# Optimization experiments

Measured on AMD Instinct MI355X. Metric: run time of the kernel, lower is better.

## Reference

```python
import jax, jax.numpy as jnp
import numpy as np

TOPK = 2
ALPHA_AUX = 0.02

def setup_inputs() -> dict:
    key = jax.random.key(0)
    ks = jax.random.split(key, 6)
    B, T, D, E, H = 2, 2048, 1024, 16, 1536
    s_in = 1.0 / np.sqrt(D)
    s_h = 1.0 / np.sqrt(H)
    return {
        "x": jax.random.normal(ks[0], (B, T, D), dtype=jnp.float32),
        "router_w": jax.random.normal(ks[1], (E, D), dtype=jnp.float32) * s_in,
        "w1": jax.random.normal(ks[2], (E, H, D), dtype=jnp.float32) * s_in,
        "b1": jax.random.normal(ks[3], (E, H), dtype=jnp.float32) * 0.01,
        "w2": jax.random.normal(ks[4], (E, D, H), dtype=jnp.float32) * s_h,
        "b2": jax.random.normal(ks[5], (E, D), dtype=jnp.float32) * 0.01,
    }

def reference(x, router_w, w1, b1, w2, b2):
    B, T, D = x.shape
    E = router_w.shape[0]
    N = B * T
    x_flat = x.reshape(N, D)

    # Router: top-k logits -> softmax gates -> dense dispatch matrix [N, E]
    logits = x_flat @ router_w.T                      # [N, E]
    vals, idx = jax.lax.top_k(logits, TOPK)           # [N, K]
    gate = jax.nn.softmax(vals, axis=-1)              # [N, K]
    rows = jnp.arange(N)[:, None]
    dispatch = jnp.zeros((N, E), dtype=x.dtype).at[rows, idx].set(gate)

    # Expert MLPs computed densely over all experts; gate==0 masks unselected,
    # reproducing the gather-MLP-scatter math exactly.
    h = jnp.einsum('nd,ehd->neh', x_flat, w1) + b1    # [N, E, H]
    h = jax.nn.gelu(h, approximate=True)              # tanh GELU
    y = jnp.einsum('neh,edh->ned', h, w2) + b2        # [N, E, D]
    out = jnp.einsum('ne,ned->nd', dispatch, y).reshape(B, T, D)

    # Auxiliary load-balancing loss
    tok_per_expert = (dispatch > 0).sum(0).astype(jnp.float32)  # [E]
    f_i = tok_per_expert / tok_per_expert.sum()
    m_i = dispatch.sum(0) / jnp.clip(tok_per_expert, 1.0, None)
    aux_loss = ALPHA_AUX * (f_i * m_i).mean()
    return out, aux_loss
```

## Files before the change

kernel.cpp:

```cpp
#include <hip/hip_runtime.h>
#include <hip/hip_bf16.h>
#include <math.h>

#define N_TOK 4096
#define DIM   1024
#define NEXP  16
#define HID   1536
#define TOPK2 2
#define NASSIGN (N_TOK * TOPK2)

#define MAX_ITEMS 80

typedef __attribute__((ext_vector_type(8))) short short8;
typedef __attribute__((ext_vector_type(4))) float floatx4;
typedef unsigned short u16;

#define GLOAD_LDS16(gp, lp)                                                     \
    __builtin_amdgcn_global_load_lds(                                           \
        (const __attribute__((address_space(1))) unsigned int*)(gp),            \
        (__attribute__((address_space(3))) unsigned int*)(lp), 16, 0, 0)

__global__ void cvt_kernel(const float* __restrict__ src, u16* __restrict__ dst, int n4) {
    int i = blockIdx.x * 256 + threadIdx.x;
    if (i >= n4) return;
    float4 v = ((const float4*)src)[i];
    __hip_bfloat16 a = __float2bfloat16(v.x), b = __float2bfloat16(v.y);
    __hip_bfloat16 c = __float2bfloat16(v.z), d = __float2bfloat16(v.w);
    ushort4 o;
    o.x = *(u16*)&a; o.y = *(u16*)&b; o.z = *(u16*)&c; o.w = *(u16*)&d;
    ((ushort4*)dst)[i] = o;
}

__global__ __launch_bounds__(256)
void logits_topk_kernel(const float* __restrict__ x, const float* __restrict__ rw,
                        int* __restrict__ idx, float* __restrict__ gate) {
    int tb = blockIdx.x * 16;
    __shared__ float xs[16][68];
    __shared__ float rs[16][68];
    __shared__ float lg[16][17];

    int tid = threadIdx.x;
    int t = tid >> 4, e = tid & 15;
    int srow = tid >> 4, scol = (tid & 15) * 4;

    float acc = 0.f;
    for (int k0 = 0; k0 < DIM; k0 += 64) {
        *(float4*)&xs[srow][scol] = *(const float4*)&x[(size_t)(tb + srow) * DIM + k0 + scol];
        *(float4*)&rs[srow][scol] = *(const float4*)&rw[(size_t)srow * DIM + k0 + scol];
        __syncthreads();
        const float2* xp = (const float2*)xs[t];
        const float2* rp = (const float2*)rs[e];
        #pragma unroll
        for (int k = 0; k < 32; k++) {
            float2 a = xp[k], b = rp[k];
            acc = fmaf(a.x, b.x, acc);
            acc = fmaf(a.y, b.y, acc);
        }
        __syncthreads();
    }
    lg[t][e] = acc;
    __syncthreads();

    if (tid < 16) {
        int n = tb + tid;
        float v0 = -3.402823466e+38f, v1 = -3.402823466e+38f;
        int i0 = 0, i1 = 0;
        #pragma unroll
        for (int ee = 0; ee < NEXP; ee++) {
            float v = lg[tid][ee];
            if (v > v0) { v1 = v0; i1 = i0; v0 = v; i0 = ee; }
            else if (v > v1) { v1 = v; i1 = ee; }
        }
        float e1 = expf(v1 - v0);
        float inv = 1.f / (1.f + e1);
        idx[2 * n] = i0; idx[2 * n + 1] = i1;
        gate[2 * n] = inv; gate[2 * n + 1] = e1 * inv;
    }
}

__global__ __launch_bounds__(256)
void plan_kernel(const int* __restrict__ idx, const float* __restrict__ gate,
                 int* __restrict__ offsets, int* __restrict__ tlist,
                 int* __restrict__ wl, int* __restrict__ wcount,
                 float* __restrict__ aux_out) {
    __shared__ int cnt_s[16];
    __shared__ float gs_s[16];
    __shared__ int pos_s[16];
    __shared__ int offs_s[17];
    int tid = threadIdx.x;
    if (tid < 16) { cnt_s[tid] = 0; gs_s[tid] = 0.f; pos_s[tid] = 0; }
    __syncthreads();
    for (int i = tid; i < NASSIGN; i += 256) {
        int e = idx[i];
        atomicAdd(&cnt_s[e], 1);
        atomicAdd(&gs_s[e], gate[i]);
    }
    __syncthreads();
    if (tid == 0) {
        int acc = 0;
        for (int e = 0; e < NEXP; e++) { offs_s[e] = acc; acc += cnt_s[e]; }
        offs_s[NEXP] = acc;
        float tot = (float)acc;
        float s = 0.f;
        for (int e = 0; e < NEXP; e++) {
            float c = (float)cnt_s[e];
            s += (c / tot) * (gs_s[e] / fmaxf(c, 1.f));
        }
        *aux_out = 0.02f * (s / (float)NEXP);
        int m = 0;
        for (int e = 0; e < NEXP; e++) {
            int nt = (cnt_s[e] + 127) >> 7;
            for (int rt = 0; rt < nt; rt++) wl[m++] = (e << 8) | rt;
        }
        *wcount = m;
    }
    __syncthreads();
    if (tid < 17) offsets[tid] = offs_s[tid];
    for (int i = tid; i < NASSIGN; i += 256) {
        int e = idx[i];
        int p = atomicAdd(&pos_s[e], 1);
        tlist[offs_s[e] + p] = i;
    }
}

__device__ __forceinline__ float gelu_tanh(float v) {
    float v3 = v * v * v;
    float t = tanhf(0.7978845608028654f * (v + 0.044715f * v3));
    return 0.5f * v * (1.f + t);
}


__global__ __launch_bounds__(256)
void gemm1_kernel(const u16* __restrict__ xb, const u16* __restrict__ w1b,
                  const float* __restrict__ b1,
                  const int* __restrict__ offsets, const int* __restrict__ tlist,
                  const int* __restrict__ wl, const int* __restrict__ wcount,
                  u16* __restrict__ h_bf) {
    int bid = blockIdx.x;
    int item = bid / 12;
    if (item >= *wcount) return;
    int colt = bid - item * 12;
    int w = wl[item];
    int e = w >> 8, rt = w & 255;
    int beg = offsets[e], ne = offsets[e + 1] - beg;
    int row0 = rt * 128, col0 = colt * 128;

    __shared__ u16 As[128 * 32];
    __shared__ u16 Bs[128 * 32];

    int tid = threadIdx.x;
    int wave = tid >> 6, lane = tid & 63;
    int wm = wave & 1, wn = wave >> 1;

    int koff = (((lane & 3) ^ ((lane >> 3) & 3)) * 8);
    const u16* aptr[2];
    const u16* bptr[2];
    #pragma unroll
    for (int q = 0; q < 2; q++) {
        int lrow = wave * 32 + q * 16 + (lane >> 2);
        int gi = beg + row0 + lrow;
        int gi2 = (row0 + lrow < ne) ? gi : beg;
        int tok = tlist[gi2] >> 1;
        aptr[q] = xb + (size_t)tok * DIM + koff;
        int n = col0 + lrow;
        bptr[q] = w1b + (size_t)(e * HID + n) * DIM + koff;
    }

    int rchunk = (((lane >> 4) ^ ((lane >> 1) & 3)) * 8);

    floatx4 acc[4][4] = {};
    for (int k0 = 0; k0 < DIM; k0 += 32) {
        #pragma unroll
        for (int q = 0; q < 2; q++) {
            GLOAD_LDS16(aptr[q] + k0, &As[(wave * 32 + q * 16) * 32]);
            GLOAD_LDS16(bptr[q] + k0, &Bs[(wave * 32 + q * 16) * 32]);
        }
        __syncthreads();
        short8 af[4], bf_[4];
        #pragma unroll
        for (int mi = 0; mi < 4; mi++)
            af[mi] = *(const short8*)&As[(wm * 64 + mi * 16 + (lane & 15)) * 32 + rchunk];
        #pragma unroll
        for (int nj = 0; nj < 4; nj++)
            bf_[nj] = *(const short8*)&Bs[(wn * 64 + nj * 16 + (lane & 15)) * 32 + rchunk];
        #pragma unroll
        for (int mi = 0; mi < 4; mi++)
            #pragma unroll
            for (int nj = 0; nj < 4; nj++)
                acc[mi][nj] = __builtin_amdgcn_mfma_f32_16x16x32_bf16(af[mi], bf_[nj], acc[mi][nj], 0, 0, 0);
        __syncthreads();
    }

    #pragma unroll
    for (int mi = 0; mi < 4; mi++) {
        #pragma unroll
        for (int r = 0; r < 4; r++) {
            int lrow = wm * 64 + mi * 16 + (lane >> 4) * 4 + r;
            if (row0 + lrow >= ne) continue;
            size_t orow = (size_t)(beg + row0 + lrow);
            #pragma unroll
            for (int nj = 0; nj < 4; nj++) {
                int col = col0 + wn * 64 + nj * 16 + (lane & 15);
                float v = acc[mi][nj][r] + b1[e * HID + col];
                __hip_bfloat16 hb = __float2bfloat16(gelu_tanh(v));
                h_bf[orow * HID + col] = *(u16*)&hb;
            }
        }
    }
}

__global__ __launch_bounds__(256)
void gemm2_kernel(const u16* __restrict__ h_bf, const u16* __restrict__ w2b,
                  const float* __restrict__ b2,
                  const int* __restrict__ offsets, const int* __restrict__ tlist,
                  const int* __restrict__ wl, const int* __restrict__ wcount,
                  const float* __restrict__ gate, float* __restrict__ out) {
    int bid = blockIdx.x;
    int item = bid >> 3;
    if (item >= *wcount) return;
    int colt = bid & 7;
    int w = wl[item];
    int e = w >> 8, rt = w & 255;
    int beg = offsets[e], ne = offsets[e + 1] - beg;
    int row0 = rt * 128, col0 = colt * 128;

    __shared__ u16 As[128 * 32];
    __shared__ u16 Bs[128 * 32];

    int tid = threadIdx.x;
    int wave = tid >> 6, lane = tid & 63;
    int wm = wave & 1, wn = wave >> 1;

    int koff = (((lane & 3) ^ ((lane >> 3) & 3)) * 8);
    const u16* aptr[2];
    const u16* bptr[2];
    #pragma unroll
    for (int q = 0; q < 2; q++) {
        int lrow = wave * 32 + q * 16 + (lane >> 2);
        int gi = beg + row0 + lrow;
        int gi2 = (row0 + lrow < ne) ? gi : beg;
        aptr[q] = h_bf + (size_t)gi2 * HID + koff;
        int n = col0 + lrow;
        bptr[q] = w2b + (size_t)(e * DIM + n) * HID + koff;
    }

    int rchunk = (((lane >> 4) ^ ((lane >> 1) & 3)) * 8);

    floatx4 acc[4][4] = {};
    for (int k0 = 0; k0 < HID; k0 += 32) {
        #pragma unroll
        for (int q = 0; q < 2; q++) {
            GLOAD_LDS16(aptr[q] + k0, &As[(wave * 32 + q * 16) * 32]);
            GLOAD_LDS16(bptr[q] + k0, &Bs[(wave * 32 + q * 16) * 32]);
        }
        __syncthreads();
        short8 af[4], bf_[4];
        #pragma unroll
        for (int mi = 0; mi < 4; mi++)
            af[mi] = *(const short8*)&As[(wm * 64 + mi * 16 + (lane & 15)) * 32 + rchunk];
        #pragma unroll
        for (int nj = 0; nj < 4; nj++)
            bf_[nj] = *(const short8*)&Bs[(wn * 64 + nj * 16 + (lane & 15)) * 32 + rchunk];
        #pragma unroll
        for (int mi = 0; mi < 4; mi++)
            #pragma unroll
            for (int nj = 0; nj < 4; nj++)
                acc[mi][nj] = __builtin_amdgcn_mfma_f32_16x16x32_bf16(af[mi], bf_[nj], acc[mi][nj], 0, 0, 0);
        __syncthreads();
    }

    #pragma unroll
    for (int mi = 0; mi < 4; mi++) {
        #pragma unroll
        for (int r = 0; r < 4; r++) {
            int lrow = wm * 64 + mi * 16 + (lane >> 4) * 4 + r;
            if (row0 + lrow >= ne) continue;
            int t = tlist[beg + row0 + lrow];
            float g = gate[t];
            int tok = t >> 1;
            #pragma unroll
            for (int nj = 0; nj < 4; nj++) {
                int col = col0 + wn * 64 + nj * 16 + (lane & 15);
                float v = g * (acc[mi][nj][r] + b2[e * DIM + col]);
                atomicAdd(&out[(size_t)tok * DIM + col], v);
            }
        }
    }
}

extern "C" void kernel_launch(void* const* d_in, const int* in_sizes, int n_in,
                              void* d_out, int out_size, void* d_ws, size_t ws_size,
                              hipStream_t stream) {
    const float* x  = (const float*)d_in[0];
    const float* rw = (const float*)d_in[1];
    const float* w1 = (const float*)d_in[2];
    const float* b1 = (const float*)d_in[3];
    const float* w2 = (const float*)d_in[4];
    const float* b2 = (const float*)d_in[5];
    float* out = (float*)d_out;

    char* ws = (char*)d_ws;
    int*   offsets = (int*)(ws + 192);
    int*   wcount  = (int*)(ws + 384);
    int*   wl      = (int*)(ws + 512);
    int*   idx     = (int*)(ws + 4096);
    float* gate    = (float*)(ws + 4096 + 4 * NASSIGN);
    int*   tlist   = (int*)(ws + 4096 + 8 * NASSIGN);
    u16*   x_bf    = (u16*)(ws + (128 << 10));
    u16*   h_bf    = x_bf + (size_t)N_TOK * DIM;
    u16*   w_bf    = h_bf + (size_t)NASSIGN * HID;

    hipMemsetAsync(d_out, 0, (size_t)out_size * 4, stream);

    cvt_kernel<<<(N_TOK * DIM / 4 + 255) / 256, 256, 0, stream>>>(x, x_bf, N_TOK * DIM / 4);
    cvt_kernel<<<(NEXP * HID * DIM / 4 + 255) / 256, 256, 0, stream>>>(w1, w_bf, NEXP * HID * DIM / 4);

    logits_topk_kernel<<<N_TOK / 16, 256, 0, stream>>>(x, rw, idx, gate);
    plan_kernel<<<1, 256, 0, stream>>>(idx, gate, offsets, tlist, wl, wcount,
                                       out + (size_t)N_TOK * DIM);

    gemm1_kernel<<<MAX_ITEMS * 12, 256, 0, stream>>>(
        x_bf, w_bf, b1, offsets, tlist, wl, wcount, h_bf);

    cvt_kernel<<<(NEXP * DIM * HID / 4 + 255) / 256, 256, 0, stream>>>(w2, w_bf, NEXP * DIM * HID / 4);

    gemm2_kernel<<<MAX_ITEMS * 8, 256, 0, stream>>>(
        h_bf, w_bf, b2, offsets, tlist, wl, wcount, gate, out);
}
```

Baseline: 455.7 us.

## Double-buffer GEMM LDS tiles, split-K gemm2, fuse x conversion into router

Both expert GEMMs now use two LDS buffers, so the next K-tile's global-to-LDS load is issued while MFMAs run on the current tile. gemm2 is split in half along the hidden dimension, doubling its block count; the bias is added only by the first half and both halves accumulate into the output atomically. The separate x-to-bf16 conversion kernel is removed and the conversion is done inside the router logits kernel, which already reads x. The cost is twice the LDS per block and twice the atomic traffic on the output in gemm2.

```diff
diff --git a/kernel.cpp b/kernel.cpp
--- a/kernel.cpp
+++ b/kernel.cpp
@@ -33,7 +33,8 @@
 
 __global__ __launch_bounds__(256)
 void logits_topk_kernel(const float* __restrict__ x, const float* __restrict__ rw,
-                        int* __restrict__ idx, float* __restrict__ gate) {
+                        int* __restrict__ idx, float* __restrict__ gate,
+                        u16* __restrict__ x_bf) {
     int tb = blockIdx.x * 16;
     __shared__ float xs[16][68];
     __shared__ float rs[16][68];
@@ -45,8 +46,16 @@
 
     float acc = 0.f;
     for (int k0 = 0; k0 < DIM; k0 += 64) {
-        *(float4*)&xs[srow][scol] = *(const float4*)&x[(size_t)(tb + srow) * DIM + k0 + scol];
+        float4 xv = *(const float4*)&x[(size_t)(tb + srow) * DIM + k0 + scol];
+        *(float4*)&xs[srow][scol] = xv;
         *(float4*)&rs[srow][scol] = *(const float4*)&rw[(size_t)srow * DIM + k0 + scol];
+        {
+            __hip_bfloat16 a = __float2bfloat16(xv.x), b = __float2bfloat16(xv.y);
+            __hip_bfloat16 c = __float2bfloat16(xv.z), d = __float2bfloat16(xv.w);
+            ushort4 o;
+            o.x = *(u16*)&a; o.y = *(u16*)&b; o.z = *(u16*)&c; o.w = *(u16*)&d;
+            *(ushort4*)&x_bf[(size_t)(tb + srow) * DIM + k0 + scol] = o;
+        }
         __syncthreads();
         const float2* xp = (const float2*)xs[t];
         const float2* rp = (const float2*)rs[e];
@@ -145,8 +154,8 @@
     int beg = offsets[e], ne = offsets[e + 1] - beg;
     int row0 = rt * 128, col0 = colt * 128;
 
-    __shared__ u16 As[128 * 32];
-    __shared__ u16 Bs[128 * 32];
+    __shared__ u16 As[2][128 * 32];
+    __shared__ u16 Bs[2][128 * 32];
 
     int tid = threadIdx.x;
     int wave = tid >> 6, lane = tid & 63;
@@ -169,26 +178,35 @@
     int rchunk = (((lane >> 4) ^ ((lane >> 1) & 3)) * 8);
 
     floatx4 acc[4][4] = {};
+    #pragma unroll
+    for (int q = 0; q < 2; q++) {
+        GLOAD_LDS16(aptr[q], &As[0][(wave * 32 + q * 16) * 32]);
+        GLOAD_LDS16(bptr[q], &Bs[0][(wave * 32 + q * 16) * 32]);
+    }
+    __syncthreads();
+    int cur = 0;
     for (int k0 = 0; k0 < DIM; k0 += 32) {
-        #pragma unroll
-        for (int q = 0; q < 2; q++) {
-            GLOAD_LDS16(aptr[q] + k0, &As[(wave * 32 + q * 16) * 32]);
-            GLOAD_LDS16(bptr[q] + k0, &Bs[(wave * 32 + q * 16) * 32]);
-        }
-        __syncthreads();
+        if (k0 + 32 < DIM) {
+            #pragma unroll
+            for (int q = 0; q < 2; q++) {
+                GLOAD_LDS16(aptr[q] + k0 + 32, &As[cur ^ 1][(wave * 32 + q * 16) * 32]);
+                GLOAD_LDS16(bptr[q] + k0 + 32, &Bs[cur ^ 1][(wave * 32 + q * 16) * 32]);
+            }
+        }
         short8 af[4], bf_[4];
         #pragma unroll
         for (int mi = 0; mi < 4; mi++)
-            af[mi] = *(const short8*)&As[(wm * 64 + mi * 16 + (lane & 15)) * 32 + rchunk];
+            af[mi] = *(const short8*)&As[cur][(wm * 64 + mi * 16 + (lane & 15)) * 32 + rchunk];
         #pragma unroll
         for (int nj = 0; nj < 4; nj++)
-            bf_[nj] = *(const short8*)&Bs[(wn * 64 + nj * 16 + (lane & 15)) * 32 + rchunk];
+            bf_[nj] = *(const short8*)&Bs[cur][(wn * 64 + nj * 16 + (lane & 15)) * 32 + rchunk];
         #pragma unroll
         for (int mi = 0; mi < 4; mi++)
             #pragma unroll
             for (int nj = 0; nj < 4; nj++)
                 acc[mi][nj] = __builtin_amdgcn_mfma_f32_16x16x32_bf16(af[mi], bf_[nj], acc[mi][nj], 0, 0, 0);
         __syncthreads();
+        cur ^= 1;
     }
 
     #pragma unroll
@@ -216,16 +234,19 @@
                   const int* __restrict__ wl, const int* __restrict__ wcount,
                   const float* __restrict__ gate, float* __restrict__ out) {
     int bid = blockIdx.x;
-    int item = bid >> 3;
+    int item = bid >> 4;
     if (item >= *wcount) return;
     int colt = bid & 7;
+    int ks = (bid >> 3) & 1;
     int w = wl[item];
     int e = w >> 8, rt = w & 255;
     int beg = offsets[e], ne = offsets[e + 1] - beg;
     int row0 = rt * 128, col0 = colt * 128;
-
-    __shared__ u16 As[128 * 32];
-    __shared__ u16 Bs[128 * 32];
+    int kbeg = ks * (HID / 2);
+    int kend = kbeg + (HID / 2);
+
+    __shared__ u16 As[2][128 * 32];
+    __shared__ u16 Bs[2][128 * 32];
 
     int tid = threadIdx.x;
     int wave = tid >> 6, lane = tid & 63;
@@ -247,26 +268,35 @@
     int rchunk = (((lane >> 4) ^ ((lane >> 1) & 3)) * 8);
 
     floatx4 acc[4][4] = {};
-    for (int k0 = 0; k0 < HID; k0 += 32) {
-        #pragma unroll
-        for (int q = 0; q < 2; q++) {
-            GLOAD_LDS16(aptr[q] + k0, &As[(wave * 32 + q * 16) * 32]);
-            GLOAD_LDS16(bptr[q] + k0, &Bs[(wave * 32 + q * 16) * 32]);
-        }
-        __syncthreads();
+    #pragma unroll
+    for (int q = 0; q < 2; q++) {
+        GLOAD_LDS16(aptr[q] + kbeg, &As[0][(wave * 32 + q * 16) * 32]);
+        GLOAD_LDS16(bptr[q] + kbeg, &Bs[0][(wave * 32 + q * 16) * 32]);
+    }
+    __syncthreads();
+    int cur = 0;
+    for (int k0 = kbeg; k0 < kend; k0 += 32) {
+        if (k0 + 32 < kend) {
+            #pragma unroll
+            for (int q = 0; q < 2; q++) {
+                GLOAD_LDS16(aptr[q] + k0 + 32, &As[cur ^ 1][(wave * 32 + q * 16) * 32]);
+                GLOAD_LDS16(bptr[q] + k0 + 32, &Bs[cur ^ 1][(wave * 32 + q * 16) * 32]);
+            }
+        }
         short8 af[4], bf_[4];
         #pragma unroll
         for (int mi = 0; mi < 4; mi++)
-            af[mi] = *(const short8*)&As[(wm * 64 + mi * 16 + (lane & 15)) * 32 + rchunk];
+            af[mi] = *(const short8*)&As[cur][(wm * 64 + mi * 16 + (lane & 15)) * 32 + rchunk];
         #pragma unroll
         for (int nj = 0; nj < 4; nj++)
-            bf_[nj] = *(const short8*)&Bs[(wn * 64 + nj * 16 + (lane & 15)) * 32 + rchunk];
+            bf_[nj] = *(const short8*)&Bs[cur][(wn * 64 + nj * 16 + (lane & 15)) * 32 + rchunk];
         #pragma unroll
         for (int mi = 0; mi < 4; mi++)
             #pragma unroll
             for (int nj = 0; nj < 4; nj++)
                 acc[mi][nj] = __builtin_amdgcn_mfma_f32_16x16x32_bf16(af[mi], bf_[nj], acc[mi][nj], 0, 0, 0);
         __syncthreads();
+        cur ^= 1;
     }
 
     #pragma unroll
@@ -281,7 +311,9 @@
             #pragma unroll
             for (int nj = 0; nj < 4; nj++) {
                 int col = col0 + wn * 64 + nj * 16 + (lane & 15);
-                float v = g * (acc[mi][nj][r] + b2[e * DIM + col]);
+                float v = acc[mi][nj][r];
+                if (ks == 0) v += b2[e * DIM + col];
+                v *= g;
                 atomicAdd(&out[(size_t)tok * DIM + col], v);
             }
         }
@@ -312,10 +344,9 @@
 
     hipMemsetAsync(d_out, 0, (size_t)out_size * 4, stream);
 
-    cvt_kernel<<<(N_TOK * DIM / 4 + 255) / 256, 256, 0, stream>>>(x, x_bf, N_TOK * DIM / 4);
     cvt_kernel<<<(NEXP * HID * DIM / 4 + 255) / 256, 256, 0, stream>>>(w1, w_bf, NEXP * HID * DIM / 4);
 
-    logits_topk_kernel<<<N_TOK / 16, 256, 0, stream>>>(x, rw, idx, gate);
+    logits_topk_kernel<<<N_TOK / 16, 256, 0, stream>>>(x, rw, idx, gate, x_bf);
     plan_kernel<<<1, 256, 0, stream>>>(idx, gate, offsets, tlist, wl, wcount,
                                        out + (size_t)N_TOK * DIM);
 
@@ -324,6 +355,6 @@
 
     cvt_kernel<<<(NEXP * DIM * HID / 4 + 255) / 256, 256, 0, stream>>>(w2, w_bf, NEXP * DIM * HID / 4);
 
-    gemm2_kernel<<<MAX_ITEMS * 8, 256, 0, stream>>>(
+    gemm2_kernel<<<MAX_ITEMS * 16, 256, 0, stream>>>(
         h_bf, w_bf, b2, offsets, tlist, wl, wcount, gate, out);
 }
```

Result: slower. 487.1 us (+6.9%).

## Fuse weight bf16 conversion into GEMMs, double-buffer LDS, replace atomics with combine

Applied to the files above, without the earlier changes.

Drops the separate fp32-to-bf16 conversion passes over w1 and w2. The GEMM kernels now load the fp32 weights directly, convert them in registers and write swizzled bf16 tiles into double-buffered shared memory, so the next tile's loads overlap the MFMA work. The conversion of x to bf16 moves into the router kernel. gemm2 writes gated per-slot outputs to a buffer, and a new combine kernel sums each token's two slots, which replaces the output memset and the float atomics. In exchange, every block re-reads and re-converts the fp32 weights, which doubles weight bytes per tile, and an extra fp32 y buffer is written and read back.

```diff
diff --git a/kernel.cpp b/kernel.cpp
--- a/kernel.cpp
+++ b/kernel.cpp
@@ -10,6 +10,8 @@
 #define NASSIGN (N_TOK * TOPK2)
 
 #define MAX_ITEMS 80
+#define G1_BLOCKS (MAX_ITEMS * 12)
+#define G2_BLOCKS (MAX_ITEMS * 8)
 
 typedef __attribute__((ext_vector_type(8))) short short8;
 typedef __attribute__((ext_vector_type(4))) float floatx4;
@@ -20,33 +22,43 @@
         (const __attribute__((address_space(1))) unsigned int*)(gp),            \
         (__attribute__((address_space(3))) unsigned int*)(lp), 16, 0, 0)
 
-__global__ void cvt_kernel(const float* __restrict__ src, u16* __restrict__ dst, int n4) {
-    int i = blockIdx.x * 256 + threadIdx.x;
-    if (i >= n4) return;
-    float4 v = ((const float4*)src)[i];
-    __hip_bfloat16 a = __float2bfloat16(v.x), b = __float2bfloat16(v.y);
-    __hip_bfloat16 c = __float2bfloat16(v.z), d = __float2bfloat16(v.w);
-    ushort4 o;
-    o.x = *(u16*)&a; o.y = *(u16*)&b; o.z = *(u16*)&c; o.w = *(u16*)&d;
-    ((ushort4*)dst)[i] = o;
+__device__ __forceinline__ u16 bf16u(float f) {
+    __hip_bfloat16 h = __float2bfloat16(f);
+    return *(u16*)&h;
+}
+
+__device__ __forceinline__ short8 cvt8(float4 a, float4 b) {
+    short8 r;
+    r[0] = (short)bf16u(a.x); r[1] = (short)bf16u(a.y);
+    r[2] = (short)bf16u(a.z); r[3] = (short)bf16u(a.w);
+    r[4] = (short)bf16u(b.x); r[5] = (short)bf16u(b.y);
+    r[6] = (short)bf16u(b.z); r[7] = (short)bf16u(b.w);
+    return r;
 }
 
 __global__ __launch_bounds__(256)
-void logits_topk_kernel(const float* __restrict__ x, const float* __restrict__ rw,
-                        int* __restrict__ idx, float* __restrict__ gate) {
+void router_kernel(const float* __restrict__ x, const float* __restrict__ rw,
+                   int* __restrict__ idx, float* __restrict__ gate,
+                   u16* __restrict__ x_bf) {
+    int tid = threadIdx.x;
     int tb = blockIdx.x * 16;
     __shared__ float xs[16][68];
     __shared__ float rs[16][68];
     __shared__ float lg[16][17];
 
-    int tid = threadIdx.x;
     int t = tid >> 4, e = tid & 15;
     int srow = tid >> 4, scol = (tid & 15) * 4;
 
     float acc = 0.f;
     for (int k0 = 0; k0 < DIM; k0 += 64) {
-        *(float4*)&xs[srow][scol] = *(const float4*)&x[(size_t)(tb + srow) * DIM + k0 + scol];
+        float4 xv = *(const float4*)&x[(size_t)(tb + srow) * DIM + k0 + scol];
+        *(float4*)&xs[srow][scol] = xv;
         *(float4*)&rs[srow][scol] = *(const float4*)&rw[(size_t)srow * DIM + k0 + scol];
+        {
+            ushort4 o;
+            o.x = bf16u(xv.x); o.y = bf16u(xv.y); o.z = bf16u(xv.z); o.w = bf16u(xv.w);
+            *(ushort4*)&x_bf[(size_t)(tb + srow) * DIM + k0 + scol] = o;
+        }
         __syncthreads();
         const float2* xp = (const float2*)xs[t];
         const float2* rp = (const float2*)rs[e];
@@ -81,6 +93,7 @@
 __global__ __launch_bounds__(256)
 void plan_kernel(const int* __restrict__ idx, const float* __restrict__ gate,
                  int* __restrict__ offsets, int* __restrict__ tlist,
+                 int* __restrict__ slot_of,
                  int* __restrict__ wl, int* __restrict__ wcount,
                  float* __restrict__ aux_out) {
     __shared__ int cnt_s[16];
@@ -119,7 +132,9 @@
     for (int i = tid; i < NASSIGN; i += 256) {
         int e = idx[i];
         int p = atomicAdd(&pos_s[e], 1);
-        tlist[offs_s[e] + p] = i;
+        int s = offs_s[e] + p;
+        tlist[s] = i;
+        slot_of[i] = s;
     }
 }
 
@@ -131,7 +146,7 @@
 
 
 __global__ __launch_bounds__(256)
-void gemm1_kernel(const u16* __restrict__ xb, const u16* __restrict__ w1b,
+void gemm1_kernel(const u16* __restrict__ xb, const float* __restrict__ w1,
                   const float* __restrict__ b1,
                   const int* __restrict__ offsets, const int* __restrict__ tlist,
                   const int* __restrict__ wl, const int* __restrict__ wcount,
@@ -145,8 +160,8 @@
     int beg = offsets[e], ne = offsets[e + 1] - beg;
     int row0 = rt * 128, col0 = colt * 128;
 
-    __shared__ u16 As[128 * 32];
-    __shared__ u16 Bs[128 * 32];
+    __shared__ u16 As[2][128 * 32];
+    __shared__ u16 Bs[2][128 * 32];
 
     int tid = threadIdx.x;
     int wave = tid >> 6, lane = tid & 63;
@@ -154,7 +169,6 @@
 
     int koff = (((lane & 3) ^ ((lane >> 3) & 3)) * 8);
     const u16* aptr[2];
-    const u16* bptr[2];
     #pragma unroll
     for (int q = 0; q < 2; q++) {
         int lrow = wave * 32 + q * 16 + (lane >> 2);
@@ -162,34 +176,61 @@
         int gi2 = (row0 + lrow < ne) ? gi : beg;
         int tok = tlist[gi2] >> 1;
         aptr[q] = xb + (size_t)tok * DIM + koff;
-        int n = col0 + lrow;
-        bptr[q] = w1b + (size_t)(e * HID + n) * DIM + koff;
-    }
+    }
+
+    int brow = tid >> 1;
+    int bh   = tid & 1;
+    const float* bsrc = w1 + (size_t)(e * HID + col0 + brow) * DIM + bh * 16;
+    int sz = (brow >> 1) & 3;
+    int bc0 = (2 * bh) ^ sz;
+    int bc1 = (2 * bh + 1) ^ sz;
 
     int rchunk = (((lane >> 4) ^ ((lane >> 1) & 3)) * 8);
 
     floatx4 acc[4][4] = {};
-    for (int k0 = 0; k0 < DIM; k0 += 32) {
-        #pragma unroll
-        for (int q = 0; q < 2; q++) {
-            GLOAD_LDS16(aptr[q] + k0, &As[(wave * 32 + q * 16) * 32]);
-            GLOAD_LDS16(bptr[q] + k0, &Bs[(wave * 32 + q * 16) * 32]);
-        }
-        __syncthreads();
+    float4 f0, f1, f2, f3;
+
+    auto STAGE_A = [&](int kt, int b) {
+        #pragma unroll
+        for (int q = 0; q < 2; q++)
+            GLOAD_LDS16(aptr[q] + kt * 32, &As[b][(wave * 32 + q * 16) * 32]);
+    };
+    auto LOAD_B = [&](int kt) {
+        const float4* p = (const float4*)(bsrc + kt * 32);
+        f0 = p[0]; f1 = p[1]; f2 = p[2]; f3 = p[3];
+    };
+    auto WRITE_B = [&](int b) {
+        *(short8*)&Bs[b][brow * 32 + bc0 * 8] = cvt8(f0, f1);
+        *(short8*)&Bs[b][brow * 32 + bc1 * 8] = cvt8(f2, f3);
+    };
+    auto CONSUME = [&](int b) {
         short8 af[4], bf_[4];
         #pragma unroll
         for (int mi = 0; mi < 4; mi++)
-            af[mi] = *(const short8*)&As[(wm * 64 + mi * 16 + (lane & 15)) * 32 + rchunk];
+            af[mi] = *(const short8*)&As[b][(wm * 64 + mi * 16 + (lane & 15)) * 32 + rchunk];
         #pragma unroll
         for (int nj = 0; nj < 4; nj++)
-            bf_[nj] = *(const short8*)&Bs[(wn * 64 + nj * 16 + (lane & 15)) * 32 + rchunk];
+            bf_[nj] = *(const short8*)&Bs[b][(wn * 64 + nj * 16 + (lane & 15)) * 32 + rchunk];
         #pragma unroll
         for (int mi = 0; mi < 4; mi++)
             #pragma unroll
             for (int nj = 0; nj < 4; nj++)
                 acc[mi][nj] = __builtin_amdgcn_mfma_f32_16x16x32_bf16(af[mi], bf_[nj], acc[mi][nj], 0, 0, 0);
+    };
+
+    const int NT = DIM / 32;
+    LOAD_B(0); STAGE_A(0, 0); WRITE_B(0);
+    __syncthreads();
+    int cur = 0;
+    for (int t = 0; t < NT - 1; ++t) {
+        LOAD_B(t + 1);
+        STAGE_A(t + 1, cur ^ 1);
+        CONSUME(cur);
+        WRITE_B(cur ^ 1);
         __syncthreads();
-    }
+        cur ^= 1;
+    }
+    CONSUME(cur);
 
     #pragma unroll
     for (int mi = 0; mi < 4; mi++) {
@@ -202,19 +243,18 @@
             for (int nj = 0; nj < 4; nj++) {
                 int col = col0 + wn * 64 + nj * 16 + (lane & 15);
                 float v = acc[mi][nj][r] + b1[e * HID + col];
-                __hip_bfloat16 hb = __float2bfloat16(gelu_tanh(v));
-                h_bf[orow * HID + col] = *(u16*)&hb;
+                h_bf[orow * HID + col] = bf16u(gelu_tanh(v));
             }
         }
     }
 }
 
 __global__ __launch_bounds__(256)
-void gemm2_kernel(const u16* __restrict__ h_bf, const u16* __restrict__ w2b,
+void gemm2_kernel(const u16* __restrict__ h_bf, const float* __restrict__ w2,
                   const float* __restrict__ b2,
                   const int* __restrict__ offsets, const int* __restrict__ tlist,
                   const int* __restrict__ wl, const int* __restrict__ wcount,
-                  const float* __restrict__ gate, float* __restrict__ out) {
+                  const float* __restrict__ gate, float* __restrict__ y) {
     int bid = blockIdx.x;
     int item = bid >> 3;
     if (item >= *wcount) return;
@@ -224,8 +264,8 @@
     int beg = offsets[e], ne = offsets[e + 1] - beg;
     int row0 = rt * 128, col0 = colt * 128;
 
-    __shared__ u16 As[128 * 32];
-    __shared__ u16 Bs[128 * 32];
+    __shared__ u16 As[2][128 * 32];
+    __shared__ u16 Bs[2][128 * 32];
 
     int tid = threadIdx.x;
     int wave = tid >> 6, lane = tid & 63;
@@ -233,41 +273,67 @@
 
     int koff = (((lane & 3) ^ ((lane >> 3) & 3)) * 8);
     const u16* aptr[2];
-    const u16* bptr[2];
     #pragma unroll
     for (int q = 0; q < 2; q++) {
         int lrow = wave * 32 + q * 16 + (lane >> 2);
         int gi = beg + row0 + lrow;
         int gi2 = (row0 + lrow < ne) ? gi : beg;
         aptr[q] = h_bf + (size_t)gi2 * HID + koff;
-        int n = col0 + lrow;
-        bptr[q] = w2b + (size_t)(e * DIM + n) * HID + koff;
-    }
+    }
+
+    int brow = tid >> 1;
+    int bh   = tid & 1;
+    const float* bsrc = w2 + (size_t)(e * DIM + col0 + brow) * HID + bh * 16;
+    int sz = (brow >> 1) & 3;
+    int bc0 = (2 * bh) ^ sz;
+    int bc1 = (2 * bh + 1) ^ sz;
 
     int rchunk = (((lane >> 4) ^ ((lane >> 1) & 3)) * 8);
 
     floatx4 acc[4][4] = {};
-    for (int k0 = 0; k0 < HID; k0 += 32) {
-        #pragma unroll
-        for (int q = 0; q < 2; q++) {
-            GLOAD_LDS16(aptr[q] + k0, &As[(wave * 32 + q * 16) * 32]);
-            GLOAD_LDS16(bptr[q] + k0, &Bs[(wave * 32 + q * 16) * 32]);
-        }
-        __syncthreads();
+    float4 f0, f1, f2, f3;
+
+    auto STAGE_A = [&](int kt, int b) {
+        #pragma unroll
+        for (int q = 0; q < 2; q++)
+            GLOAD_LDS16(aptr[q] + kt * 32, &As[b][(wave * 32 + q * 16) * 32]);
+    };
+    auto LOAD_B = [&](int kt) {
+        const float4* p = (const float4*)(bsrc + kt * 32);
+        f0 = p[0]; f1 = p[1]; f2 = p[2]; f3 = p[3];
+    };
+    auto WRITE_B = [&](int b) {
+        *(short8*)&Bs[b][brow * 32 + bc0 * 8] = cvt8(f0, f1);
+        *(short8*)&Bs[b][brow * 32 + bc1 * 8] = cvt8(f2, f3);
+    };
+    auto CONSUME = [&](int b) {
         short8 af[4], bf_[4];
         #pragma unroll
         for (int mi = 0; mi < 4; mi++)
-            af[mi] = *(const short8*)&As[(wm * 64 + mi * 16 + (lane & 15)) * 32 + rchunk];
+            af[mi] = *(const short8*)&As[b][(wm * 64 + mi * 16 + (lane & 15)) * 32 + rchunk];
         #pragma unroll
         for (int nj = 0; nj < 4; nj++)
-            bf_[nj] = *(const short8*)&Bs[(wn * 64 + nj * 16 + (lane & 15)) * 32 + rchunk];
+            bf_[nj] = *(const short8*)&Bs[b][(wn * 64 + nj * 16 + (lane & 15)) * 32 + rchunk];
         #pragma unroll
         for (int mi = 0; mi < 4; mi++)
             #pragma unroll
             for (int nj = 0; nj < 4; nj++)
                 acc[mi][nj] = __builtin_amdgcn_mfma_f32_16x16x32_bf16(af[mi], bf_[nj], acc[mi][nj], 0, 0, 0);
+    };
+
+    const int NT = HID / 32;
+    LOAD_B(0); STAGE_A(0, 0); WRITE_B(0);
+    __syncthreads();
+    int cur = 0;
+    for (int t = 0; t < NT - 1; ++t) {
+        LOAD_B(t + 1);
+        STAGE_A(t + 1, cur ^ 1);
+        CONSUME(cur);
+        WRITE_B(cur ^ 1);
         __syncthreads();
-    }
+        cur ^= 1;
+    }
+    CONSUME(cur);
 
     #pragma unroll
     for (int mi = 0; mi < 4; mi++) {
@@ -275,17 +341,30 @@
         for (int r = 0; r < 4; r++) {
             int lrow = wm * 64 + mi * 16 + (lane >> 4) * 4 + r;
             if (row0 + lrow >= ne) continue;
-            int t = tlist[beg + row0 + lrow];
+            int slot = beg + row0 + lrow;
+            int t = tlist[slot];
             float g = gate[t];
-            int tok = t >> 1;
             #pragma unroll
             for (int nj = 0; nj < 4; nj++) {
                 int col = col0 + wn * 64 + nj * 16 + (lane & 15);
                 float v = g * (acc[mi][nj][r] + b2[e * DIM + col]);
-                atomicAdd(&out[(size_t)tok * DIM + col], v);
+                y[(size_t)slot * DIM + col] = v;
             }
         }
     }
+}
+
+__global__ __launch_bounds__(256)
+void combine_kernel(const float* __restrict__ y, const int* __restrict__ slot_of,
+                    float* __restrict__ out) {
+    int t = blockIdx.x;
+    int c4 = threadIdx.x;
+    int s0 = slot_of[2 * t], s1 = slot_of[2 * t + 1];
+    float4 a = ((const float4*)(y + (size_t)s0 * DIM))[c4];
+    float4 b = ((const float4*)(y + (size_t)s1 * DIM))[c4];
+    float4 o;
+    o.x = a.x + b.x; o.y = a.y + b.y; o.z = a.z + b.z; o.w = a.w + b.w;
+    ((float4*)(out + (size_t)t * DIM))[c4] = o;
 }
 
 extern "C" void kernel_launch(void* const* d_in, const int* in_sizes, int n_in,
@@ -306,24 +385,17 @@
     int*   idx     = (int*)(ws + 4096);
     float* gate    = (float*)(ws + 4096 + 4 * NASSIGN);
     int*   tlist   = (int*)(ws + 4096 + 8 * NASSIGN);
-    u16*   x_bf    = (u16*)(ws + (128 << 10));
+    int*   slot_of = (int*)(ws + 4096 + 12 * NASSIGN);
+    u16*   x_bf    = (u16*)(ws + (256 << 10));
     u16*   h_bf    = x_bf + (size_t)N_TOK * DIM;
-    u16*   w_bf    = h_bf + (size_t)NASSIGN * HID;
-
-    hipMemsetAsync(d_out, 0, (size_t)out_size * 4, stream);
-
-    cvt_kernel<<<(N_TOK * DIM / 4 + 255) / 256, 256, 0, stream>>>(x, x_bf, N_TOK * DIM / 4);
-    cvt_kernel<<<(NEXP * HID * DIM / 4 + 255) / 256, 256, 0, stream>>>(w1, w_bf, NEXP * HID * DIM / 4);
-
-    logits_topk_kernel<<<N_TOK / 16, 256, 0, stream>>>(x, rw, idx, gate);
-    plan_kernel<<<1, 256, 0, stream>>>(idx, gate, offsets, tlist, wl, wcount,
-                                       out + (size_t)N_TOK * DIM);
-
-    gemm1_kernel<<<MAX_ITEMS * 12, 256, 0, stream>>>(
-        x_bf, w_bf, b1, offsets, tlist, wl, wcount, h_bf);
-
-    cvt_kernel<<<(NEXP * DIM * HID / 4 + 255) / 256, 256, 0, stream>>>(w2, w_bf, NEXP * DIM * HID / 4);
-
-    gemm2_kernel<<<MAX_ITEMS * 8, 256, 0, stream>>>(
-        h_bf, w_bf, b2, offsets, tlist, wl, wcount, gate, out);
-}
+    float* y       = (float*)(h_bf + (size_t)NASSIGN * HID);
+
+    router_kernel<<<N_TOK / 16, 256, 0, stream>>>(x, rw, idx, gate, x_bf);
+    plan_kernel<<<1, 256, 0, stream>>>(idx, gate, offsets, tlist, slot_of,
+                                       wl, wcount, out + (size_t)N_TOK * DIM);
+    gemm1_kernel<<<G1_BLOCKS, 256, 0, stream>>>(
+        x_bf, w1, b1, offsets, tlist, wl, wcount, h_bf);
+    gemm2_kernel<<<G2_BLOCKS, 256, 0, stream>>>(
+        h_bf, w2, b2, offsets, tlist, wl, wcount, gate, y);
+    combine_kernel<<<N_TOK, 256, 0, stream>>>(y, slot_of, out);
+}
```

Result: no change. 456.7 us (+0.2%).
